# Kernel optimization log

Hardware: AMD Instinct MI355X
Metric: run time of the kernel (lower is better)

The kernel has to match this reference:

```python
import jax, jax.numpy as jnp
import numpy as np

B, D, H, NS = 64, 2048, 4096, 25  # batch, x_dim (num_links), n_hidden=2*x_dim, n_steps


def setup_inputs() -> dict:
    key = jax.random.key(0)
    ks = jax.random.split(key, 12)
    # binary half-masks per leapfrog step (faithful to _construct_masks with np_seed=1)
    rng = np.random.RandomState(1)
    masks = np.zeros((NS, D), np.float32)
    for i in range(NS):
        idx = rng.permutation(D)[: D // 2]
        masks[i, idx] = 1.0
    # sinusoidal time encoding per step (_construct_time)
    ts = np.stack([
        [np.cos(2 * np.pi * i / NS), np.sin(2 * np.pi * i / NS)] for i in range(NS)
    ]).astype(np.float32)

    def lin(k, shape, fan_in):
        return jax.random.normal(k, shape, jnp.float32) / np.sqrt(fan_in)

    return dict(
        position=jax.random.normal(ks[0], (B, D), jnp.float32),
        momentum_f=jax.random.normal(ks[1], (B, D), jnp.float32),
        momentum_b=jax.random.normal(ks[2], (B, D), jnp.float32),
        u_dir=jax.random.uniform(ks[3], (B,), jnp.float32),
        u_accept=jax.random.uniform(ks[4], (B,), jnp.float32),
        eps=jnp.full((1,), 0.1, jnp.float32),
        masks=jnp.asarray(masks),
        ts=jnp.asarray(ts),
        # stacked params for the two GenericNets: [0]=position_fn, [1]=momentum_fn
        W1=lin(ks[5], (2, D, H), D), W2=lin(ks[6], (2, D, H), D),
        Wt=lin(ks[7], (2, 2, H), 2), b1=jnp.zeros((2, H), jnp.float32),
        Wh=lin(ks[8], (2, H, H), H), bh=jnp.zeros((2, H), jnp.float32),
        Ws=lin(ks[9], (2, H, D), H), bs=jnp.zeros((2, D), jnp.float32),
        cs=jnp.zeros((2, D), jnp.float32),
        Wtr=lin(ks[10], (2, H, D), H), btr=jnp.zeros((2, D), jnp.float32),
        Wq=lin(ks[11], (2, H, D), H), bq=jnp.zeros((2, D), jnp.float32),
        cq=jnp.zeros((2, D), jnp.float32),
    )


def reference(position, momentum_f, momentum_b, u_dir, u_accept, eps, masks, ts,
              W1, W2, Wt, b1, Wh, bh, Ws, bs, cs, Wtr, btr, Wq, bq, cq):
    e = eps[0]
    POS, MOM = 0, 1

    def net(n, a, b, t):
        # GenericNet: two-hidden-layer MLP emitting (scale S, translation T, transformation Q)
        h = jax.nn.relu(a @ W1[n] + b @ W2[n] + t @ Wt[n] + b1[n])
        h = jax.nn.relu(h @ Wh[n] + bh[n])
        S = jnp.tanh(h @ Ws[n] + bs[n]) * jnp.exp(cs[n])
        T = h @ Wtr[n] + btr[n]
        Q = jnp.tanh(h @ Wq[n] + bq[n]) * jnp.exp(cq[n])
        return S, T, Q

    def potential(x):              # U(1) gauge-style action: sum(1 - cos(x))
        return jnp.sum(1.0 - jnp.cos(x), axis=1)

    def grad_potential(x):
        return jnp.sin(x)

    def hamiltonian(x, v):
        return potential(x) + 0.5 * jnp.sum(v * v, axis=1)

    def mom_fwd(pos, mom, t):
        g = grad_potential(pos)
        S, T, Q = net(MOM, pos, g, t)
        sc, tr = 0.5 * e * S, e * Q
        mom = mom * jnp.exp(sc) - 0.5 * e * (jnp.exp(tr) * g - T)
        return mom, jnp.sum(sc, axis=1)

    def pos_fwd(pos, mom, t, m, minv):
        S, T, Q = net(POS, mom, m * pos, t)
        sc, tr = e * S, e * Q
        pos = m * pos + minv * (pos * jnp.exp(sc) + e * (jnp.exp(tr) * mom + T))
        return pos, jnp.sum(minv * sc, axis=1)

    def mom_bwd(pos, mom, t):
        g = grad_potential(pos)
        S, T, Q = net(MOM, pos, g, t)
        sc, tr = -0.5 * e * S, e * Q
        mom = jnp.exp(sc) * (mom + 0.5 * e * (jnp.exp(tr) * g - T))
        return mom, jnp.sum(sc, axis=1)

    def pos_bwd(pos, mom, t, m, minv):
        S, T, Q = net(POS, mom, m * pos, t)
        sc, tr = e * S, e * Q
        pos = m * pos + minv * jnp.exp(sc) * (pos - e * (jnp.exp(tr) * mom + T))
        return pos, jnp.sum(minv * sc, axis=1)

    def step_fwd(carry, xs):
        pos, mom, sld = carry
        m, t = xs
        t = t[None, :]
        minv = 1.0 - m
        mom, ld = mom_fwd(pos, mom, t); sld = sld + ld
        pos, ld = pos_fwd(pos, mom, t, m, minv); sld = sld + ld
        pos, ld = pos_fwd(pos, mom, t, minv, m); sld = sld + ld
        mom, ld = mom_fwd(pos, mom, t); sld = sld + ld
        return (pos, mom, sld), None

    def step_bwd(carry, xs):
        pos, mom, sld = carry
        m, t = xs
        t = t[None, :]
        minv = 1.0 - m
        mom, ld = mom_bwd(pos, mom, t); sld = sld + ld
        pos, ld = pos_bwd(pos, mom, t, minv, m); sld = sld + ld
        pos, ld = pos_bwd(pos, mom, t, m, minv); sld = sld + ld
        mom, ld = mom_bwd(pos, mom, t); sld = sld + ld
        return (pos, mom, sld), None

    zero = jnp.zeros(position.shape[0], position.dtype)
    (pf, mf, sldf), _ = jax.lax.scan(step_fwd, (position, momentum_f, zero), (masks, ts))
    (pb, mb, sldb), _ = jax.lax.scan(step_bwd, (position, momentum_b, zero), (masks[::-1], ts[::-1]))

    def accept_prob(mom0, pos1, mom1, sld):
        d = hamiltonian(position, mom0) - hamiltonian(pos1, mom1) + sld
        p = jnp.exp(jnp.minimum(d, 0.0))
        return jnp.where(jnp.isfinite(p), p, jnp.zeros_like(p))

    apf = accept_prob(momentum_f, pf, mf, sldf)
    apb = accept_prob(momentum_b, pb, mb, sldb)

    fmask = (u_dir > 0.5).astype(position.dtype)
    bmask = 1.0 - fmask
    position_post = fmask[:, None] * pf + bmask[:, None] * pb
    momentum_post = fmask[:, None] * mf + bmask[:, None] * mb
    ap = fmask * apf + bmask * apb
    amask = (ap > u_accept).astype(position.dtype)
    position_out = amask[:, None] * position_post + (1.0 - amask)[:, None] * position
    return position_post, momentum_post, ap, position_out
```

## Files before the change

### kernel.cpp

```cpp
#include <hip/hip_runtime.h>

#define BD   64
#define DD   2048
#define HH   4096
#define NSS  25
#define BBr  128

typedef _Float16 halfx8 __attribute__((ext_vector_type(8)));
typedef float    floatx4 __attribute__((ext_vector_type(4)));

__device__ __forceinline__ unsigned short f2h_bits(float x) {
    union { _Float16 h; unsigned short u; } c;
    c.h = (_Float16)x;
    return c.u;
}

__global__ void init_kernel(const float* __restrict__ position,
                            const float* __restrict__ momf,
                            const float* __restrict__ momb,
                            float* __restrict__ pos, float* __restrict__ mom,
                            float* __restrict__ sld,
                            unsigned short* __restrict__ Abuf) {
    int idx = blockIdx.x * 256 + threadIdx.x;
    int r = idx >> 11, d = idx & 2047;
    float p = position[((r & 63) << 11) + d];
    pos[idx] = p;
    mom[idx] = (r < 64) ? momf[(r << 11) + d] : momb[((r - 64) << 11) + d];
    Abuf[(r << 12) + d]        = f2h_bits(p);
    Abuf[(r << 12) + 2048 + d] = f2h_bits(sinf(p));
    if (idx < BBr) sld[idx] = 0.f;
}

__global__ __launch_bounds__(256) void transpose_cvt_kernel(
        const float* __restrict__ src, int ldi,
        unsigned short* __restrict__ dst, int ldo) {
    __shared__ float tile[32][33];
    const int rb = blockIdx.y * 32;
    const int cb = blockIdx.x * 32;
    const int t  = threadIdx.x;
    const int r  = t >> 3;
    const int c4 = (t & 7) * 4;
    float4 v = *reinterpret_cast<const float4*>(src + (size_t)(rb + r) * ldi + cb + c4);
    tile[r][c4 + 0] = v.x; tile[r][c4 + 1] = v.y;
    tile[r][c4 + 2] = v.z; tile[r][c4 + 3] = v.w;
    __syncthreads();
    union { unsigned short us[4]; uint2 v; } pk;
#pragma unroll
    for (int j = 0; j < 4; ++j) pk.us[j] = f2h_bits(tile[c4 + j][r]);
    *reinterpret_cast<uint2*>(dst + (size_t)(cb + r) * ldo + rb + c4) = pk.v;
}

template <int EPI>
__global__ __launch_bounds__(256) void gemm_bt_kernel(
        const unsigned short* __restrict__ A, int lda, int K,
        const unsigned short* __restrict__ BT,
        void* __restrict__ Cout, int ldc,
        const float* __restrict__ biasp, const float* __restrict__ Wtn,
        const float* __restrict__ ts, int sF, int sB) {
    const int lane = threadIdx.x & 63;
    const int wave = threadIdx.x >> 6;
    const int fl   = lane & 15;
    const int qd   = lane >> 4;
    const int bn   = blockIdx.x * 16;

    const unsigned short* pa0 = A  + (size_t)(wave * 32 + fl) * lda + qd * 8;
    const unsigned short* pa1 = pa0 + (size_t)16 * lda;
    const unsigned short* pb  = BT + (size_t)(bn + fl) * K + qd * 8;

    floatx4 acc0 = {0.f, 0.f, 0.f, 0.f};
    floatx4 acc1 = {0.f, 0.f, 0.f, 0.f};

    for (int k0 = 0; k0 < K; k0 += 128) {
#pragma unroll
        for (int u = 0; u < 4; ++u) {
            halfx8 a0 = *reinterpret_cast<const halfx8*>(pa0 + u * 32);
            halfx8 a1 = *reinterpret_cast<const halfx8*>(pa1 + u * 32);
            halfx8 b  = *reinterpret_cast<const halfx8*>(pb  + u * 32);
            acc0 = __builtin_amdgcn_mfma_f32_16x16x32_f16(a0, b, acc0, 0, 0, 0);
            acc1 = __builtin_amdgcn_mfma_f32_16x16x32_f16(a1, b, acc1, 0, 0, 0);
        }
        pa0 += 128; pa1 += 128; pb += 128;
    }

    const int col = bn + fl;
#pragma unroll
    for (int fn = 0; fn < 2; ++fn) {
        floatx4 a = (fn == 0) ? acc0 : acc1;
        const int row_base = wave * 32 + fn * 16 + qd * 4;
#pragma unroll
        for (int rr = 0; rr < 4; ++rr) {
            int row = row_base + rr;
            float v = a[rr];
            if (EPI == 0) {
                int sidx = (row < 64) ? sF : sB;
                v += biasp[col] + ts[2 * sidx] * Wtn[col] + ts[2 * sidx + 1] * Wtn[HH + col];
                v = fmaxf(v, 0.f);
                ((unsigned short*)Cout)[(size_t)row * ldc + col] = f2h_bits(v);
            } else if (EPI == 1) {
                v = fmaxf(v + biasp[col], 0.f);
                ((unsigned short*)Cout)[(size_t)row * ldc + col] = f2h_bits(v);
            } else {
                ((float*)Cout)[(size_t)row * ldc + col] = v;
            }
        }
    }
}

template <int BMODE, int EPI>
__global__ __launch_bounds__(256) void gemm_kernel(
        const unsigned short* __restrict__ A, int lda, int K,
        const float* __restrict__ Bp0, const float* __restrict__ Bp1,
        const float* __restrict__ Bp2, int ldb,
        void* __restrict__ Cout, int ldc,
        const float* __restrict__ biasp, const float* __restrict__ Wtn,
        const float* __restrict__ ts, int sF, int sB) {
    __shared__ unsigned short As[32][40];
    __shared__ unsigned short Bs[64][40];

    const int tid  = threadIdx.x;
    const int wave = tid >> 6;
    const int lane = tid & 63;
    const int fl   = lane & 15;
    const int qd   = lane >> 4;
    const int bm   = blockIdx.y * 32;
    const int bn   = blockIdx.x * 64;
    const int wm   = (wave >> 1) * 16;
    const int wn   = (wave & 1) * 32;

    const int ar = tid >> 3;
    const int ak = (tid & 7) * 4;
    const int kloc = wave * 8;
    const int bnl  = lane;

    floatx4 acc0 = {0.f, 0.f, 0.f, 0.f};
    floatx4 acc1 = {0.f, 0.f, 0.f, 0.f};

    for (int k0 = 0; k0 < K; k0 += 32) {
        *reinterpret_cast<uint2*>(&As[ar][ak]) =
            *reinterpret_cast<const uint2*>(A + (size_t)(bm + ar) * lda + k0 + ak);

        float fv[8];
        if (BMODE == 0) {
            int kk = k0 + kloc;
            const float* base = (kk < 2048) ? (Bp0 + (size_t)kk * ldb)
                                            : (Bp1 + (size_t)(kk - 2048) * ldb);
            base += bn + bnl;
#pragma unroll
            for (int j = 0; j < 8; ++j) fv[j] = base[(size_t)j * ldb];
        } else if (BMODE == 1) {
            const float* base = Bp0 + (size_t)(k0 + kloc) * ldb + bn + bnl;
#pragma unroll
            for (int j = 0; j < 8; ++j) fv[j] = base[(size_t)j * ldb];
        } else {
            int third = bn >> 11;
            const float* Bsel = (third == 0) ? Bp0 : ((third == 1) ? Bp1 : Bp2);
            const float* base = Bsel + (size_t)(k0 + kloc) * ldb + (bn - (third << 11)) + bnl;
#pragma unroll
            for (int j = 0; j < 8; ++j) fv[j] = base[(size_t)j * ldb];
        }
        union { unsigned short us[8]; uint4 v; } pk;
#pragma unroll
        for (int j = 0; j < 8; ++j) pk.us[j] = f2h_bits(fv[j]);
        *reinterpret_cast<uint4*>(&Bs[bnl][kloc]) = pk.v;

        __syncthreads();

        halfx8 afr = *reinterpret_cast<const halfx8*>(&As[wm + fl][qd * 8]);
        halfx8 bf0 = *reinterpret_cast<const halfx8*>(&Bs[wn + fl][qd * 8]);
        halfx8 bf1 = *reinterpret_cast<const halfx8*>(&Bs[wn + 16 + fl][qd * 8]);
        acc0 = __builtin_amdgcn_mfma_f32_16x16x32_f16(afr, bf0, acc0, 0, 0, 0);
        acc1 = __builtin_amdgcn_mfma_f32_16x16x32_f16(afr, bf1, acc1, 0, 0, 0);

        __syncthreads();
    }

    const int row0 = bm + wm + qd * 4;
#pragma unroll
    for (int fn = 0; fn < 2; ++fn) {
        floatx4 a = (fn == 0) ? acc0 : acc1;
        int col = bn + wn + fn * 16 + fl;
#pragma unroll
        for (int rr = 0; rr < 4; ++rr) {
            int row = row0 + rr;
            float v = a[rr];
            if (EPI == 0) {
                int sidx = (row < 64) ? sF : sB;
                v += biasp[col] + ts[2 * sidx] * Wtn[col] + ts[2 * sidx + 1] * Wtn[HH + col];
                v = fmaxf(v, 0.f);
                ((unsigned short*)Cout)[(size_t)row * ldc + col] = f2h_bits(v);
            } else if (EPI == 1) {
                v = fmaxf(v + biasp[col], 0.f);
                ((unsigned short*)Cout)[(size_t)row * ldc + col] = f2h_bits(v);
            } else {
                ((float*)Cout)[(size_t)row * ldc + col] = v;
            }
        }
    }
}

__device__ __forceinline__ void block_reduce_atomic(float v, float* dst) {
    for (int off = 32; off; off >>= 1) v += __shfl_down(v, off, 64);
    __shared__ float red[4];
    if ((threadIdx.x & 63) == 0) red[threadIdx.x >> 6] = v;
    __syncthreads();
    if (threadIdx.x == 0) atomicAdd(dst, red[0] + red[1] + red[2] + red[3]);
}

__global__ void update_mom_kernel(const float* __restrict__ pos, float* __restrict__ mom,
                                  float* __restrict__ sld, const float* __restrict__ STQ,
                                  const float* __restrict__ bs, const float* __restrict__ cs,
                                  const float* __restrict__ btr, const float* __restrict__ bq,
                                  const float* __restrict__ cq, const float* __restrict__ eps,
                                  const float* __restrict__ masks, int sF, int sB,
                                  int writeNext, unsigned short* __restrict__ Abuf) {
    int r = blockIdx.y;
    int d = blockIdx.x * 256 + threadIdx.x;
    float e = eps[0];
    size_t ro = (size_t)r * 6144;
    float S = tanhf(STQ[ro + d] + bs[d]) * expf(cs[d]);
    float T = STQ[ro + 2048 + d] + btr[d];
    float Q = tanhf(STQ[ro + 4096 + d] + bq[d]) * expf(cq[d]);
    size_t idx = (size_t)r * 2048 + d;
    float p = pos[idx], v = mom[idx];
    float g = sinf(p);
    float tr = e * Q, sc;
    if (r < 64) { sc = 0.5f * e * S;  v = v * expf(sc) - 0.5f * e * (expf(tr) * g - T); }
    else        { sc = -0.5f * e * S; v = expf(sc) * (v + 0.5f * e * (expf(tr) * g - T)); }
    mom[idx] = v;
    if (writeNext) {
        float m2 = (r < 64) ? masks[sF * 2048 + d] : 1.f - masks[sB * 2048 + d];
        Abuf[(r << 12) + d]        = f2h_bits(v);
        Abuf[(r << 12) + 2048 + d] = f2h_bits(m2 * p);
    }
    block_reduce_atomic(sc, sld + r);
}

__global__ void update_pos_kernel(float* __restrict__ pos, const float* __restrict__ mom,
                                  float* __restrict__ sld, const float* __restrict__ STQ,
                                  const float* __restrict__ bs, const float* __restrict__ cs,
                                  const float* __restrict__ btr, const float* __restrict__ bq,
                                  const float* __restrict__ cq, const float* __restrict__ eps,
                                  const float* __restrict__ masks, int sF, int sB, int sub,
                                  unsigned short* __restrict__ Abuf) {
    int r = blockIdx.y;
    int d = blockIdx.x * 256 + threadIdx.x;
    float e = eps[0];
    size_t ro = (size_t)r * 6144;
    float S = tanhf(STQ[ro + d] + bs[d]) * expf(cs[d]);
    float T = STQ[ro + 2048 + d] + btr[d];
    float Q = tanhf(STQ[ro + 4096 + d] + bq[d]) * expf(cq[d]);
    size_t idx = (size_t)r * 2048 + d;
    float p = pos[idx], v = mom[idx];
    float sc = e * S, tr = e * Q;
    float mf = masks[sF * 2048 + d], mb = masks[sB * 2048 + d];
    float pn, ld;
    if (r < 64) {
        float m  = (sub == 2) ? mf : 1.f - mf;
        float mi = 1.f - m;
        pn = m * p + mi * (p * expf(sc) + e * (expf(tr) * v + T));
        ld = mi * sc;
    } else {
        float m  = (sub == 2) ? 1.f - mb : mb;
        float mi = 1.f - m;
        pn = m * p + mi * expf(sc) * (p - e * (expf(tr) * v + T));
        ld = mi * sc;
    }
    pos[idx] = pn;
    if (sub == 2) {
        float m3 = (r < 64) ? 1.f - mf : mb;
        Abuf[(r << 12) + d]        = f2h_bits(v);
        Abuf[(r << 12) + 2048 + d] = f2h_bits(m3 * pn);
    } else {
        Abuf[(r << 12) + d]        = f2h_bits(pn);
        Abuf[(r << 12) + 2048 + d] = f2h_bits(sinf(pn));
    }
    block_reduce_atomic(ld, sld + r);
}

__global__ void accept_kernel(const float* __restrict__ position,
                              const float* __restrict__ momf, const float* __restrict__ momb,
                              const float* __restrict__ pos, const float* __restrict__ mom,
                              const float* __restrict__ sld, float* __restrict__ ap_all) {
    int r = blockIdx.x;
    int rb = r & 63;
    const float* m0 = (r < 64) ? (momf + (size_t)rb * 2048) : (momb + (size_t)rb * 2048);
    float s = 0.f;
    for (int d = threadIdx.x; d < 2048; d += 256) {
        float x0 = position[rb * 2048 + d];
        float v0 = m0[d];
        float x1 = pos[(size_t)r * 2048 + d];
        float v1 = mom[(size_t)r * 2048 + d];
        s += (cosf(x1) - cosf(x0)) + 0.5f * (v0 * v0 - v1 * v1);
    }
    for (int off = 32; off; off >>= 1) s += __shfl_down(s, off, 64);
    __shared__ float red[4];
    if ((threadIdx.x & 63) == 0) red[threadIdx.x >> 6] = s;
    __syncthreads();
    if (threadIdx.x == 0) {
        float dd = red[0] + red[1] + red[2] + red[3] + sld[r];
        float p = isnan(dd) ? 0.f : expf(dd < 0.f ? dd : 0.f);
        if (!isfinite(p)) p = 0.f;
        ap_all[r] = p;
    }
}

__global__ void combine_kernel(const float* __restrict__ position,
                               const float* __restrict__ u_dir, const float* __restrict__ u_accept,
                               const float* __restrict__ pos, const float* __restrict__ mom,
                               const float* __restrict__ ap_all, float* __restrict__ out) {
    int idx = blockIdx.x * 256 + threadIdx.x;
    int b = idx >> 11, d = idx & 2047;
    float fm = (u_dir[b] > 0.5f) ? 1.f : 0.f;
    float pf = pos[(size_t)b * 2048 + d],       pb = pos[(size_t)(64 + b) * 2048 + d];
    float mf = mom[(size_t)b * 2048 + d],       mb = mom[(size_t)(64 + b) * 2048 + d];
    float ppost = fm * pf + (1.f - fm) * pb;
    float mpost = fm * mf + (1.f - fm) * mb;
    float ap = fm * ap_all[b] + (1.f - fm) * ap_all[64 + b];
    float am = (ap > u_accept[b]) ? 1.f : 0.f;
    out[idx] = ppost;
    out[131072 + idx] = mpost;
    if (d == 0) out[262144 + b] = ap;
    out[262208 + idx] = am * ppost + (1.f - am) * position[idx];
}

extern "C" void kernel_launch(void* const* d_in, const int* in_sizes, int n_in,
                              void* d_out, int out_size, void* d_ws, size_t ws_size,
                              hipStream_t stream) {
    const float* position   = (const float*)d_in[0];
    const float* momentum_f = (const float*)d_in[1];
    const float* momentum_b = (const float*)d_in[2];
    const float* u_dir      = (const float*)d_in[3];
    const float* u_accept   = (const float*)d_in[4];
    const float* eps        = (const float*)d_in[5];
    const float* masks      = (const float*)d_in[6];
    const float* ts         = (const float*)d_in[7];
    const float* W1         = (const float*)d_in[8];
    const float* W2         = (const float*)d_in[9];
    const float* Wt         = (const float*)d_in[10];
    const float* b1         = (const float*)d_in[11];
    const float* Wh         = (const float*)d_in[12];
    const float* bh         = (const float*)d_in[13];
    const float* Ws         = (const float*)d_in[14];
    const float* bs         = (const float*)d_in[15];
    const float* cs         = (const float*)d_in[16];
    const float* Wtr        = (const float*)d_in[17];
    const float* btr        = (const float*)d_in[18];
    const float* Wq         = (const float*)d_in[19];
    const float* bq         = (const float*)d_in[20];
    const float* cq         = (const float*)d_in[21];
    float* out = (float*)d_out;

    float* pos    = (float*)d_ws;
    float* mom    = pos + BBr * DD;
    float* sld    = mom + BBr * DD;
    float* ap_all = sld + BBr;
    float* STQ    = ap_all + BBr;
    unsigned short* Abuf = (unsigned short*)(STQ + BBr * 3 * DD);
    unsigned short* h1   = Abuf + (size_t)BBr * 2 * DD;
    unsigned short* h2   = h1 + (size_t)BBr * HH;
    unsigned short* BTw  = h2 + (size_t)BBr * HH;

    const size_t BT1sz = (size_t)HH * 2 * DD;
    const size_t BThsz = (size_t)HH * HH;
    const size_t BT3sz = (size_t)3 * DD * HH;
    const size_t perNet = BT1sz + BThsz + BT3sz;
    unsigned short* BT1[2] = { BTw,                 BTw + perNet };
    unsigned short* BTh[2] = { BTw + BT1sz,         BTw + perNet + BT1sz };
    unsigned short* BT3[2] = { BTw + BT1sz + BThsz, BTw + perNet + BT1sz + BThsz };

    const size_t NEED = (size_t)((char*)(BTw + 2 * perNet) - (char*)d_ws);
    const bool fast = (ws_size >= NEED);

    const size_t DH  = (size_t)DD * HH;
    const size_t HH2 = (size_t)HH * HH;

    init_kernel<<<BBr * DD / 256, 256, 0, stream>>>(position, momentum_f, momentum_b,
                                                    pos, mom, sld, Abuf);

    if (fast) {
        for (int n = 0; n < 2; ++n) {
            transpose_cvt_kernel<<<dim3(HH / 32, DD / 32), 256, 0, stream>>>(
                W1 + n * DH, HH, BT1[n], 2 * DD);
            transpose_cvt_kernel<<<dim3(HH / 32, DD / 32), 256, 0, stream>>>(
                W2 + n * DH, HH, BT1[n] + DD, 2 * DD);
            transpose_cvt_kernel<<<dim3(HH / 32, HH / 32), 256, 0, stream>>>(
                Wh + n * HH2, HH, BTh[n], HH);
            transpose_cvt_kernel<<<dim3(DD / 32, HH / 32), 256, 0, stream>>>(
                Ws + n * DH, DD, BT3[n], HH);
            transpose_cvt_kernel<<<dim3(DD / 32, HH / 32), 256, 0, stream>>>(
                Wtr + n * DH, DD, BT3[n] + (size_t)DD * HH, HH);
            transpose_cvt_kernel<<<dim3(DD / 32, HH / 32), 256, 0, stream>>>(
                Wq + n * DH, DD, BT3[n] + (size_t)2 * DD * HH, HH);
        }
    }

    for (int i = 0; i < NSS; ++i) {
        int sF = i, sB = NSS - 1 - i;
        for (int subidx = 0; subidx < 4; ++subidx) {
            bool isMom = (subidx == 0 || subidx == 3);
            int n = isMom ? 1 : 0;
            int sub = (subidx == 1) ? 2 : 3;

            if (fast) {
                gemm_bt_kernel<0><<<HH / 16, 256, 0, stream>>>(
                    Abuf, 2 * DD, 2 * DD, BT1[n], h1, HH,
                    b1 + n * HH, Wt + n * 2 * HH, ts, sF, sB);
                gemm_bt_kernel<1><<<HH / 16, 256, 0, stream>>>(
                    h1, HH, HH, BTh[n], h2, HH,
                    bh + n * HH, nullptr, ts, sF, sB);
                gemm_bt_kernel<2><<<3 * DD / 16, 256, 0, stream>>>(
                    h2, HH, HH, BT3[n], STQ, 3 * DD,
                    nullptr, nullptr, ts, sF, sB);
            } else {
                gemm_kernel<0, 0><<<dim3(HH / 64, 4), 256, 0, stream>>>(
                    Abuf, 2 * DD, 2 * DD,
                    W1 + n * DH, W2 + n * DH, nullptr, HH, h1, HH,
                    b1 + n * HH, Wt + n * 2 * HH, ts, sF, sB);
                gemm_kernel<1, 1><<<dim3(HH / 64, 4), 256, 0, stream>>>(
                    h1, HH, HH, Wh + n * HH2, nullptr, nullptr, HH, h2, HH,
                    bh + n * HH, nullptr, ts, sF, sB);
                gemm_kernel<2, 2><<<dim3(3 * DD / 64, 4), 256, 0, stream>>>(
                    h2, HH, HH, Ws + n * DH, Wtr + n * DH, Wq + n * DH, DD, STQ, 3 * DD,
                    nullptr, nullptr, ts, sF, sB);
            }

            if (isMom)
                update_mom_kernel<<<dim3(DD / 256, BBr), 256, 0, stream>>>(
                    pos, mom, sld, STQ, bs + DD, cs + DD, btr + DD, bq + DD, cq + DD,
                    eps, masks, sF, sB, (subidx == 0) ? 1 : 0, Abuf);
            else
                update_pos_kernel<<<dim3(DD / 256, BBr), 256, 0, stream>>>(
                    pos, mom, sld, STQ, bs, cs, btr, bq, cq, eps, masks, sF, sB, sub, Abuf);
        }
    }

    accept_kernel<<<BBr, 256, 0, stream>>>(position, momentum_f, momentum_b,
                                           pos, mom, sld, ap_all);
    combine_kernel<<<BD * DD / 256, 256, 0, stream>>>(position, u_dir, u_accept,
                                                      pos, mom, ap_all, out);
}
```

Measured before the change: 19.97 ms.

## Stage GEMM A/B tiles through double-buffered swizzled LDS with register prefetch

Replaces the direct-from-global MFMA GEMM with a version that loads 128-wide K chunks of A (128 rows) and B (16 rows) cooperatively into XOR-swizzled shared memory. It double-buffers the chunks and prefetches the next one into registers while the MFMAs run on the current one. The aim is coalesced global loads and hiding their latency behind compute. In exchange it uses about 72KB of LDS per block, which limits occupancy, and adds one barrier per K chunk.

Result: slower. 30.05 ms (+50.5%).

```diff
diff --git a/kernel.cpp b/kernel.cpp
--- a/kernel.cpp
+++ b/kernel.cpp
@@ -51,42 +51,87 @@
 }
 
 template <int EPI>
-__global__ __launch_bounds__(256) void gemm_bt_kernel(
+__global__ __launch_bounds__(256) void gemm_lds_kernel(
         const unsigned short* __restrict__ A, int lda, int K,
         const unsigned short* __restrict__ BT,
         void* __restrict__ Cout, int ldc,
         const float* __restrict__ biasp, const float* __restrict__ Wtn,
         const float* __restrict__ ts, int sF, int sB) {
-    const int lane = threadIdx.x & 63;
-    const int wave = threadIdx.x >> 6;
-    const int fl   = lane & 15;
-    const int qd   = lane >> 4;
+    __shared__ unsigned short lds[2 * 18432];
+
+    const int tid  = threadIdx.x;
+    const int w    = tid >> 6;
+    const int lane = tid & 63;
+    const int hi   = lane >> 4;
+    const int lo   = lane & 15;
+    const int fq   = lo & 7;
     const int bn   = blockIdx.x * 16;
 
-    const unsigned short* pa0 = A  + (size_t)(wave * 32 + fl) * lda + qd * 8;
-    const unsigned short* pa1 = pa0 + (size_t)16 * lda;
-    const unsigned short* pb  = BT + (size_t)(bn + fl) * K + qd * 8;
+    const int als = tid & 15;
+    const int arg = tid >> 4;
+    const int brow = tid >> 4;
+    const int bls  = tid & 15;
+
+    const unsigned short* gA = A + als * 8;
+    const unsigned short* gB = BT + (size_t)(bn + brow) * K + bls * 8;
 
     floatx4 acc0 = {0.f, 0.f, 0.f, 0.f};
     floatx4 acc1 = {0.f, 0.f, 0.f, 0.f};
 
-    for (int k0 = 0; k0 < K; k0 += 128) {
+    const int nch = K >> 7;
+
+    uint4 ar[8];
+    uint4 br;
+
+#pragma unroll
+    for (int i = 0; i < 8; ++i)
+        ar[i] = *reinterpret_cast<const uint4*>(gA + (size_t)(arg * 8 + i) * lda);
+    br = *reinterpret_cast<const uint4*>(gB);
+#pragma unroll
+    for (int i = 0; i < 8; ++i)
+        *reinterpret_cast<uint4*>(&lds[(arg * 8 + i) * 128 + ((als ^ i) << 3)]) = ar[i];
+    *reinterpret_cast<uint4*>(&lds[16384 + brow * 128 + ((bls ^ (brow & 7)) << 3)]) = br;
+    __syncthreads();
+
+    const int ra0 = (32 * w + lo) * 128;
+    const int rb0 = 16384 + lo * 128;
+
+    for (int t = 0; t < nch; ++t) {
+        if (t + 1 < nch) {
+            const unsigned short* ga = gA + (size_t)(t + 1) * 128;
+            const unsigned short* gb = gB + (size_t)(t + 1) * 128;
+#pragma unroll
+            for (int i = 0; i < 8; ++i)
+                ar[i] = *reinterpret_cast<const uint4*>(ga + (size_t)(arg * 8 + i) * lda);
+            br = *reinterpret_cast<const uint4*>(gb);
+        }
+
+        const unsigned short* Lb = lds + (t & 1) * 18432;
 #pragma unroll
         for (int u = 0; u < 4; ++u) {
-            halfx8 a0 = *reinterpret_cast<const halfx8*>(pa0 + u * 32);
-            halfx8 a1 = *reinterpret_cast<const halfx8*>(pa1 + u * 32);
-            halfx8 b  = *reinterpret_cast<const halfx8*>(pb  + u * 32);
+            const int ph = ((hi + 4 * u) ^ fq) << 3;
+            halfx8 a0 = *reinterpret_cast<const halfx8*>(Lb + ra0 + ph);
+            halfx8 a1 = *reinterpret_cast<const halfx8*>(Lb + ra0 + 2048 + ph);
+            halfx8 b  = *reinterpret_cast<const halfx8*>(Lb + rb0 + ph);
             acc0 = __builtin_amdgcn_mfma_f32_16x16x32_f16(a0, b, acc0, 0, 0, 0);
             acc1 = __builtin_amdgcn_mfma_f32_16x16x32_f16(a1, b, acc1, 0, 0, 0);
         }
-        pa0 += 128; pa1 += 128; pb += 128;
-    }
-
-    const int col = bn + fl;
+
+        if (t + 1 < nch) {
+            unsigned short* Ln = lds + ((t + 1) & 1) * 18432;
+#pragma unroll
+            for (int i = 0; i < 8; ++i)
+                *reinterpret_cast<uint4*>(&Ln[(arg * 8 + i) * 128 + ((als ^ i) << 3)]) = ar[i];
+            *reinterpret_cast<uint4*>(&Ln[16384 + brow * 128 + ((bls ^ (brow & 7)) << 3)]) = br;
+        }
+        __syncthreads();
+    }
+
+    const int col = bn + lo;
 #pragma unroll
     for (int fn = 0; fn < 2; ++fn) {
         floatx4 a = (fn == 0) ? acc0 : acc1;
-        const int row_base = wave * 32 + fn * 16 + qd * 4;
+        const int row_base = w * 32 + fn * 16 + hi * 4;
 #pragma unroll
         for (int rr = 0; rr < 4; ++rr) {
             int row = row_base + rr;
@@ -402,13 +447,13 @@
             int sub = (subidx == 1) ? 2 : 3;
 
             if (fast) {
-                gemm_bt_kernel<0><<<HH / 16, 256, 0, stream>>>(
+                gemm_lds_kernel<0><<<HH / 16, 256, 0, stream>>>(
                     Abuf, 2 * DD, 2 * DD, BT1[n], h1, HH,
                     b1 + n * HH, Wt + n * 2 * HH, ts, sF, sB);
-                gemm_bt_kernel<1><<<HH / 16, 256, 0, stream>>>(
+                gemm_lds_kernel<1><<<HH / 16, 256, 0, stream>>>(
                     h1, HH, HH, BTh[n], h2, HH,
                     bh + n * HH, nullptr, ts, sF, sB);
-                gemm_bt_kernel<2><<<3 * DD / 16, 256, 0, stream>>>(
+                gemm_lds_kernel<2><<<3 * DD / 16, 256, 0, stream>>>(
                     h2, HH, HH, BT3[n], STQ, 3 * DD,
                     nullptr, nullptr, ts, sF, sB);
             } else {
```

## Split K across waves in weight GEMMs with shared-memory reduction

Applied to the files above, without the earlier changes.

Adds intra-block split-K to the MFMA GEMM kernel. Each block now runs 4x (or 2x) more waves, each handling a slice of K, and the partial accumulators are summed through LDS before the epilogue. The goal is more memory-level parallelism and more waves in flight for these skinny, weight-bandwidth-bound GEMMs (M=128), which previously had only 256 or 384 blocks of 4 waves. The cost is extra LDS traffic, a block-wide barrier, and larger blocks.

Result: faster. 18.79 ms (-5.9%).

```diff
diff --git a/kernel.cpp b/kernel.cpp
--- a/kernel.cpp
+++ b/kernel.cpp
@@ -50,27 +50,30 @@
     *reinterpret_cast<uint2*>(dst + (size_t)(cb + r) * ldo + rb + c4) = pk.v;
 }
 
-template <int EPI>
-__global__ __launch_bounds__(256) void gemm_bt_kernel(
+template <int EPI, int KS>
+__global__ __launch_bounds__(KS * 256, 4) void gemm_bt_kernel(
         const unsigned short* __restrict__ A, int lda, int K,
         const unsigned short* __restrict__ BT,
         void* __restrict__ Cout, int ldc,
         const float* __restrict__ biasp, const float* __restrict__ Wtn,
         const float* __restrict__ ts, int sF, int sB) {
-    const int lane = threadIdx.x & 63;
-    const int wave = threadIdx.x >> 6;
+    const int tid  = threadIdx.x;
+    const int lane = tid & 63;
+    const int mw   = (tid >> 6) & 3;
+    const int kq   = tid >> 8;
     const int fl   = lane & 15;
     const int qd   = lane >> 4;
     const int bn   = blockIdx.x * 16;
 
-    const unsigned short* pa0 = A  + (size_t)(wave * 32 + fl) * lda + qd * 8;
+    const int Kq = K / KS;
+    const unsigned short* pa0 = A + (size_t)(mw * 32 + fl) * lda + kq * Kq + qd * 8;
     const unsigned short* pa1 = pa0 + (size_t)16 * lda;
-    const unsigned short* pb  = BT + (size_t)(bn + fl) * K + qd * 8;
+    const unsigned short* pb  = BT + (size_t)(bn + fl) * K + kq * Kq + qd * 8;
 
     floatx4 acc0 = {0.f, 0.f, 0.f, 0.f};
     floatx4 acc1 = {0.f, 0.f, 0.f, 0.f};
 
-    for (int k0 = 0; k0 < K; k0 += 128) {
+    for (int k0 = 0; k0 < Kq; k0 += 128) {
 #pragma unroll
         for (int u = 0; u < 4; ++u) {
             halfx8 a0 = *reinterpret_cast<const halfx8*>(pa0 + u * 32);
@@ -82,11 +85,26 @@
         pa0 += 128; pa1 += 128; pb += 128;
     }
 
+    __shared__ float red[(KS - 1) * 4][64][8];
+    if (kq > 0) {
+        float* p = &red[(kq - 1) * 4 + mw][lane][0];
+#pragma unroll
+        for (int j = 0; j < 4; ++j) { p[j] = acc0[j]; p[j + 4] = acc1[j]; }
+    }
+    __syncthreads();
+    if (kq != 0) return;
+#pragma unroll
+    for (int q = 0; q < KS - 1; ++q) {
+        const float* p = &red[q * 4 + mw][lane][0];
+#pragma unroll
+        for (int j = 0; j < 4; ++j) { acc0[j] += p[j]; acc1[j] += p[j + 4]; }
+    }
+
     const int col = bn + fl;
 #pragma unroll
     for (int fn = 0; fn < 2; ++fn) {
         floatx4 a = (fn == 0) ? acc0 : acc1;
-        const int row_base = wave * 32 + fn * 16 + qd * 4;
+        const int row_base = mw * 32 + fn * 16 + qd * 4;
 #pragma unroll
         for (int rr = 0; rr < 4; ++rr) {
             int row = row_base + rr;
@@ -402,13 +420,13 @@
             int sub = (subidx == 1) ? 2 : 3;
 
             if (fast) {
-                gemm_bt_kernel<0><<<HH / 16, 256, 0, stream>>>(
+                gemm_bt_kernel<0, 4><<<HH / 16, 1024, 0, stream>>>(
                     Abuf, 2 * DD, 2 * DD, BT1[n], h1, HH,
                     b1 + n * HH, Wt + n * 2 * HH, ts, sF, sB);
-                gemm_bt_kernel<1><<<HH / 16, 256, 0, stream>>>(
+                gemm_bt_kernel<1, 4><<<HH / 16, 1024, 0, stream>>>(
                     h1, HH, HH, BTh[n], h2, HH,
                     bh + n * HH, nullptr, ts, sF, sB);
-                gemm_bt_kernel<2><<<3 * DD / 16, 256, 0, stream>>>(
+                gemm_bt_kernel<2, 2><<<3 * DD / 16, 512, 0, stream>>>(
                     h2, HH, HH, BT3[n], STQ, 3 * DD,
                     nullptr, nullptr, ts, sF, sB);
             } else {
```
